# Kernel optimization log

Measured on AMD Instinct MI355X. Metric: run time of the kernel, lower is better.

The kernel has to match this reference:

```python
import jax, jax.numpy as jnp
import numpy as np

OUT = 7          # pooler output_size
RATIO = 2        # sampling_ratio
MIN_LEVEL, MAX_LEVEL = 2, 5
CANON_SIZE, CANON_LEVEL = 224.0, 4.0
SCALES = (0.25, 0.125, 0.0625, 0.03125)


def setup_inputs() -> dict:
    key = jax.random.key(0)
    ks = jax.random.split(key, 8)
    feat2 = jax.random.normal(ks[0], (2, 256, 200, 304), dtype=jnp.float32)
    feat3 = jax.random.normal(ks[1], (2, 256, 100, 152), dtype=jnp.float32)
    feat4 = jax.random.normal(ks[2], (2, 256, 50, 76), dtype=jnp.float32)
    feat5 = jax.random.normal(ks[3], (2, 256, 25, 38), dtype=jnp.float32)
    M = 1000
    imH, imW = 800.0, 1216.0
    cx = jax.random.uniform(ks[4], (M,)) * imW
    cy = jax.random.uniform(ks[5], (M,)) * imH
    wh = jax.random.uniform(ks[6], (M, 2)) * 400.0 + 8.0  # box sizes 8..408 px -> spans levels 2..5
    x0 = jnp.clip(cx - wh[:, 0] / 2, 0.0, imW - 1.0)
    x1 = jnp.clip(cx + wh[:, 0] / 2, 1.0, imW)
    y0 = jnp.clip(cy - wh[:, 1] / 2, 0.0, imH - 1.0)
    y1 = jnp.clip(cy + wh[:, 1] / 2, 1.0, imH)
    boxes = jnp.stack([x0, y0, x1, y1], axis=1).astype(jnp.float32)
    batch_idx = jax.random.randint(ks[7], (M,), 0, 2, dtype=jnp.int32)
    return {"feat2": feat2, "feat3": feat3, "feat4": feat4, "feat5": feat5,
            "boxes": boxes, "batch_idx": batch_idx}


def _assign_levels(boxes):
    # detectron2 assign_boxes_to_levels
    area = (boxes[:, 2] - boxes[:, 0]) * (boxes[:, 3] - boxes[:, 1])
    size = jnp.sqrt(area)
    lvl = jnp.floor(CANON_LEVEL + jnp.log2(size / CANON_SIZE + 1e-8))
    lvl = jnp.clip(lvl, MIN_LEVEL, MAX_LEVEL)
    return (lvl - MIN_LEVEL).astype(jnp.int32)  # [M] in 0..3


def _axis_weights(c, size):
    # torchvision roi_align bilinear clamping (per axis, separable)
    valid = ((c >= -1.0) & (c <= size)).astype(c.dtype)
    cc = jnp.maximum(c, 0.0)
    lo_f = jnp.floor(cc)
    cap = lo_f >= size - 1
    lo = jnp.where(cap, size - 1, lo_f).astype(jnp.int32)
    hi = jnp.where(cap, size - 1, lo + 1).astype(jnp.int32)
    l = jnp.where(cap, 0.0, cc - lo_f)
    return lo, hi, (1.0 - l) * valid, l * valid


def _roi_align(feat, boxes, bidx, scale):
    # feat [N,C,H,W], boxes [M,4] xyxy, aligned=True (ROIAlignV2)
    N, C, H, W = feat.shape
    M = boxes.shape[0]
    b = boxes * scale - 0.5  # aligned: shift by -0.5 after scaling
    x0, y0 = b[:, 0], b[:, 1]
    bin_w = (b[:, 2] - x0) / OUT
    bin_h = (b[:, 3] - y0) / OUT
    S = OUT * RATIO
    s = np.arange(S)
    offs = jnp.asarray((s // RATIO) + ((s % RATIO) + 0.5) / RATIO, dtype=feat.dtype)  # [S]
    ys = y0[:, None] + bin_h[:, None] * offs[None, :]  # [M,S]
    xs = x0[:, None] + bin_w[:, None] * offs[None, :]  # [M,S]
    ylo, yhi, wyl, wyh = _axis_weights(ys, H)
    xlo, xhi, wxl, wxh = _axis_weights(xs, W)

    def gather(yi, xi):
        # -> [M, S, S, C]
        return feat[bidx[:, None, None], :, yi[:, :, None], xi[:, None, :]]

    val = (gather(ylo, xlo) * (wyl[:, :, None] * wxl[:, None, :])[..., None]
         + gather(ylo, xhi) * (wyl[:, :, None] * wxh[:, None, :])[..., None]
         + gather(yhi, xlo) * (wyh[:, :, None] * wxl[:, None, :])[..., None]
         + gather(yhi, xhi) * (wyh[:, :, None] * wxh[:, None, :])[..., None])
    # average over the RATIOxRATIO sample subgrid of each output bin
    val = val.reshape(M, OUT, RATIO, OUT, RATIO, C).mean(axis=(2, 4))
    return val.transpose(0, 3, 1, 2)  # [M, C, OUT, OUT]


def reference(feat2, feat3, feat4, feat5, boxes, batch_idx):
    feats = (feat2, feat3, feat4, feat5)
    assign = _assign_levels(boxes)  # [M]
    M, C = boxes.shape[0], feat2.shape[1]
    out = jnp.zeros((M, C, OUT, OUT), dtype=feat2.dtype)
    for lvl, (f, sc) in enumerate(zip(feats, SCALES)):
        pooled = _roi_align(f, boxes, batch_idx, sc)
        out = out + pooled * (assign == lvl)[:, None, None, None].astype(out.dtype)
    return out
```

## Files before the change

kernel.cpp:

```cpp
#include <hip/hip_runtime.h>


#define NCH 256
#define POOL 7
#define NBIN 49
#define NSAMP 14
#define CAP 1152
#define WPB 4

typedef __attribute__((address_space(3))) void       as3_void;
typedef __attribute__((address_space(1))) const void as1_void;

__global__ __launch_bounds__(256, 8) void roi_align_kernel(
    const float* __restrict__ f0, const float* __restrict__ f1,
    const float* __restrict__ f2, const float* __restrict__ f3,
    const float* __restrict__ boxes, const int* __restrict__ bidx,
    float* __restrict__ out, int M)
{
    __shared__ float sF[WPB][CAP];
    __shared__ int   sXlo[WPB][NSAMP], sXhi[WPB][NSAMP];
    __shared__ int   sYlo[WPB][NSAMP], sYhi[WPB][NSAMP];
    __shared__ float sWxl[WPB][NSAMP], sWxh[WPB][NSAMP];
    __shared__ float sWyl[WPB][NSAMP], sWyh[WPB][NSAMP];

    const int lane = threadIdx.x & 63;
    const int w    = __builtin_amdgcn_readfirstlane(threadIdx.x >> 6);
    const int unit = blockIdx.x * WPB + w;
    if (unit >= M * NCH) return;
    const int m = unit >> 8;
    const int c = unit & (NCH - 1);

    float bx0 = boxes[4 * m + 0];
    float by0 = boxes[4 * m + 1];
    float bx1 = boxes[4 * m + 2];
    float by1 = boxes[4 * m + 3];

    float area = (bx1 - bx0) * (by1 - by0);
    float sz   = sqrtf(area);
    float lvlf = floorf(4.0f + log2f(sz / 224.0f + 1e-8f));
    lvlf = fminf(fmaxf(lvlf, 2.0f), 5.0f);
    int lvl = (int)lvlf - 2;

    const float* fp; int H; int W; float scale;
    if (lvl == 0)      { fp = f0; H = 200; W = 304; scale = 0.25f;    }
    else if (lvl == 1) { fp = f1; H = 100; W = 152; scale = 0.125f;   }
    else if (lvl == 2) { fp = f2; H = 50;  W = 76;  scale = 0.0625f;  }
    else               { fp = f3; H = 25;  W = 38;  scale = 0.03125f; }

    float x0 = bx0 * scale - 0.5f;
    float y0 = by0 * scale - 0.5f;
    float bin_w = (bx1 * scale - 0.5f - x0) * (1.0f / 7.0f);
    float bin_h = (by1 * scale - 0.5f - y0) * (1.0f / 7.0f);

    if (lane < 2 * NSAMP) {
        int axis = lane >= NSAMP;
        int s    = axis ? (lane - NSAMP) : lane;
        float off = (float)(s >> 1) + ((s & 1) ? 0.75f : 0.25f);
        float cv    = axis ? (y0 + bin_h * off) : (x0 + bin_w * off);
        float size  = axis ? (float)H : (float)W;
        float valid = (cv >= -1.0f && cv <= size) ? 1.0f : 0.0f;
        float cc    = fmaxf(cv, 0.0f);
        float lo_f  = floorf(cc);
        bool  cap   = lo_f >= size - 1.0f;
        int   lo    = cap ? (int)size - 1 : (int)lo_f;
        int   hi    = cap ? lo : lo + 1;
        float l     = cap ? 0.0f : (cc - lo_f);
        float wlo   = (1.0f - l) * valid;
        float whi   = l * valid;
        if (axis) { sYlo[w][s] = lo; sYhi[w][s] = hi;
                    sWyl[w][s] = wlo; sWyh[w][s] = whi; }
        else      { sXlo[w][s] = lo; sXhi[w][s] = hi;
                    sWxl[w][s] = wlo; sWxh[w][s] = whi; }
    }

    const int rx0 = sXlo[w][0];
    const int ry0 = sYlo[w][0];
    const int FW  = sXhi[w][NSAMP - 1] - rx0 + 1;
    const int FH  = sYhi[w][NSAMP - 1] - ry0 + 1;
    const int lpr = (FW + 3) >> 2;
    const int RS4 = lpr << 2;

    const size_t HW = (size_t)(H * W);
    const float* src  = fp + ((size_t)bidx[m] * NCH + c) * HW
                           + (size_t)ry0 * W + rx0;
    const float* fend = fp + (size_t)2 * NCH * HW;

    bool safe16 = (src + (size_t)(FH - 1) * W + RS4 <= fend)
               && (FH * RS4 <= CAP);

    if (safe16) {
        int rpi   = 64 / lpr;
        int iters = (FH + rpi - 1) / rpi;
        int sfy   = lane / lpr;
        int sfx4  = (lane - sfy * lpr) << 2;
        if (sfy < rpi) {
            const float* g    = src + (size_t)sfy * W + sfx4;
            const float* gmax = src + (size_t)(FH - 1) * W + sfx4;
            const size_t gstep = (size_t)rpi * W;
            char* lbase = (char*)&sF[w][0];
            const unsigned lstep = (unsigned)(rpi * RS4) * 4u;
            for (int it = 0; it < iters; ++it) {
                const float* gc = (g > gmax) ? gmax : g;
                __builtin_amdgcn_global_load_lds((as1_void*)gc,
                                                 (as3_void*)lbase, 16, 0, 0);
                g += gstep;
                lbase += lstep;
            }
        }
    } else {
        int fh2 = FH;
        if (fh2 * RS4 > CAP) fh2 = CAP / RS4;
        for (int i = lane; i < fh2 * RS4; i += 64) {
            int fy = i / RS4;
            int fx = i - fy * RS4;
            int cx = fx < FW ? fx : (FW - 1);
            sF[w][i] = src[(size_t)fy * W + cx];
        }
    }

    __builtin_amdgcn_s_waitcnt(0);
    __asm__ __volatile__("" ::: "memory");

    if (lane < NBIN) {
        int py = lane / POOL;
        int px = lane - POOL * py;
        int xa = 2 * px, xb = xa + 1;
        int xr0 = sXlo[w][xa] - rx0;
        int xr1 = sXlo[w][xb] - rx0;
        int xp0 = min(xr0 + 1, FW - 1);
        int xp1 = min(xr1 + 1, FW - 1);
        float wxl0 = sWxl[w][xa], wxh0 = sWxh[w][xa];
        float wxl1 = sWxl[w][xb], wxh1 = sWxh[w][xb];
        const float* Fb = &sF[w][0];
        float acc = 0.0f;
        #pragma unroll
        for (int sy = 0; sy < 2; ++sy) {
            int ysi = 2 * py + sy;
            int yl = sYlo[w][ysi] - ry0;
            int yh = sYhi[w][ysi] - ry0;
            float wl = sWyl[w][ysi], wh = sWyh[w][ysi];
            const float* rl = Fb + yl * RS4;
            const float* rh = Fb + yh * RS4;
            float s0 = rl[xr0] * wxl0 + rl[xp0] * wxh0
                     + rl[xr1] * wxl1 + rl[xp1] * wxh1;
            float s1 = rh[xr0] * wxl0 + rh[xp0] * wxh0
                     + rh[xr1] * wxl1 + rh[xp1] * wxh1;
            acc += wl * s0 + wh * s1;
        }
        out[(size_t)unit * NBIN + lane] = acc * 0.25f;
    }
}

extern "C" void kernel_launch(void* const* d_in, const int* in_sizes, int n_in,
                              void* d_out, int out_size, void* d_ws, size_t ws_size,
                              hipStream_t stream) {
    const float* f0    = (const float*)d_in[0];
    const float* f1    = (const float*)d_in[1];
    const float* f2    = (const float*)d_in[2];
    const float* f3    = (const float*)d_in[3];
    const float* boxes = (const float*)d_in[4];
    const int*   bidx  = (const int*)d_in[5];
    float* out = (float*)d_out;

    int M = in_sizes[4] / 4;
    int units = M * NCH;
    int blocks = (units + WPB - 1) / WPB;
    hipLaunchKernelGGL(roi_align_kernel, dim3(blocks), dim3(256), 0, stream,
                       f0, f1, f2, f3, boxes, bidx, out, M);
}
```

Baseline: 298.8 us.

## Precompute per-ROI sampling tables in a separate kernel shared by all channels

Adds a small precompute kernel that computes, once per ROI, the level, base offset, load geometry, magic-number divisors and per-sample indices and weights into a workspace table. The main kernel then reads this table instead of redoing the box math and LDS table writes for each of the 256 channels. It also switches to 32-bit offset arithmetic and multiply-shift division. The cost is an extra kernel launch plus table reads from global memory in every wave.

```diff
diff --git a/kernel.cpp b/kernel.cpp
--- a/kernel.cpp
+++ b/kernel.cpp
@@ -4,24 +4,127 @@
 #define NCH 256
 #define POOL 7
 #define NBIN 49
-#define NSAMP 14
 #define CAP 1152
 #define WPB 4
+#define TS 128
 
 typedef __attribute__((address_space(3))) void       as3_void;
 typedef __attribute__((address_space(1))) const void as1_void;
+
+__global__ __launch_bounds__(256) void roi_precompute_kernel(
+    const float* __restrict__ boxes, const int* __restrict__ bidx,
+    unsigned int* __restrict__ tab, int M)
+{
+    const int lane = threadIdx.x & 63;
+    const int m = blockIdx.x * WPB + (threadIdx.x >> 6);
+    if (m >= M) return;
+
+    float bx0 = boxes[4 * m + 0];
+    float by0 = boxes[4 * m + 1];
+    float bx1 = boxes[4 * m + 2];
+    float by1 = boxes[4 * m + 3];
+
+    float area = (bx1 - bx0) * (by1 - by0);
+    float sz   = sqrtf(area);
+    float lvlf = floorf(4.0f + log2f(sz / 224.0f + 1e-8f));
+    lvlf = fminf(fmaxf(lvlf, 2.0f), 5.0f);
+    int lvl = (int)lvlf - 2;
+
+    int H, W; float scale;
+    if (lvl == 0)      { H = 200; W = 304; scale = 0.25f;    }
+    else if (lvl == 1) { H = 100; W = 152; scale = 0.125f;   }
+    else if (lvl == 2) { H = 50;  W = 76;  scale = 0.0625f;  }
+    else               { H = 25;  W = 38;  scale = 0.03125f; }
+
+    float x0 = bx0 * scale - 0.5f;
+    float y0 = by0 * scale - 0.5f;
+    float bin_w = (bx1 * scale - 0.5f - x0) * (1.0f / 7.0f);
+    float bin_h = (by1 * scale - 0.5f - y0) * (1.0f / 7.0f);
+
+    int axis = lane >= 14;
+    int s    = axis ? (lane - 14) : lane;
+    float off = (float)(s >> 1) + ((s & 1) ? 0.75f : 0.25f);
+    float cv    = axis ? (y0 + bin_h * off) : (x0 + bin_w * off);
+    float size  = axis ? (float)H : (float)W;
+    float valid = (cv >= -1.0f && cv <= size) ? 1.0f : 0.0f;
+    float cc    = fmaxf(cv, 0.0f);
+    float lo_f  = floorf(cc);
+    bool  capd  = lo_f >= size - 1.0f;
+    int   lo    = capd ? (int)size - 1 : (int)lo_f;
+    int   hi    = capd ? lo : lo + 1;
+    float l     = capd ? 0.0f : (cc - lo_f);
+    float wlo   = (1.0f - l) * valid;
+    float whi   = l * valid;
+
+    int rx0 = __shfl(lo, 0);
+    int rxe = __shfl(hi, 13);
+    int ry0 = __shfl(lo, 14);
+    int rye = __shfl(hi, 27);
+
+    int FW  = rxe - rx0 + 1;
+    int FH  = rye - ry0 + 1;
+    int lpr = (FW + 3) >> 2;
+    int RS4 = lpr << 2;
+    int rpi = 64 / lpr;
+    int iters = (FH + rpi - 1) / rpi;
+    unsigned Mg  = (65536u   + (unsigned)lpr - 1u) / (unsigned)lpr;
+    unsigned Mg2 = (4194304u + (unsigned)RS4 - 1u) / (unsigned)RS4;
+    unsigned HW  = (unsigned)(H * W);
+    unsigned base_off = (unsigned)bidx[m] * 256u * HW
+                      + (unsigned)ry0 * (unsigned)W + (unsigned)rx0;
+    int FH2 = FH;
+    if (FH2 * RS4 > CAP) FH2 = CAP / RS4;
+    unsigned lastoff = base_off + 255u * HW
+                     + (unsigned)(FH - 1) * (unsigned)W + (unsigned)RS4;
+    int safe = (lastoff <= 2u * 256u * HW) && (FH * RS4 <= CAP);
+
+    unsigned* t = tab + (size_t)m * TS;
+    if (lane == 0) {
+        t[0]  = base_off;
+        t[1]  = (unsigned)lvl;
+        t[2]  = HW;
+        t[3]  = (unsigned)W;
+        t[4]  = (unsigned)lpr;
+        t[5]  = Mg;
+        t[6]  = (unsigned)rpi;
+        t[7]  = (unsigned)iters;
+        t[8]  = (unsigned)(rpi * W);
+        t[9]  = (unsigned)((rpi * RS4) << 2);
+        t[10] = (unsigned)((FH - 1) * W);
+        t[11] = (unsigned)safe;
+        t[12] = (unsigned)FW;
+        t[13] = (unsigned)RS4;
+        t[14] = (unsigned)FH2;
+        t[15] = Mg2;
+    }
+    if (lane < 28) {
+        if (!axis) {
+            int xr = lo - rx0;
+            int xp = min(xr + 1, FW - 1);
+            uint4 v;
+            v.x = (unsigned)xr;
+            v.y = (unsigned)xp;
+            v.z = __float_as_uint(wlo);
+            v.w = __float_as_uint(whi);
+            *(uint4*)(t + 16 + 4 * s) = v;
+        } else {
+            uint4 v;
+            v.x = (unsigned)((lo - ry0) * RS4);
+            v.y = (unsigned)((hi - ry0) * RS4);
+            v.z = __float_as_uint(wlo);
+            v.w = __float_as_uint(whi);
+            *(uint4*)(t + 72 + 4 * s) = v;
+        }
+    }
+}
 
 __global__ __launch_bounds__(256, 8) void roi_align_kernel(
     const float* __restrict__ f0, const float* __restrict__ f1,
     const float* __restrict__ f2, const float* __restrict__ f3,
-    const float* __restrict__ boxes, const int* __restrict__ bidx,
+    const unsigned int* __restrict__ tab,
     float* __restrict__ out, int M)
 {
     __shared__ float sF[WPB][CAP];
-    __shared__ int   sXlo[WPB][NSAMP], sXhi[WPB][NSAMP];
-    __shared__ int   sYlo[WPB][NSAMP], sYhi[WPB][NSAMP];
-    __shared__ float sWxl[WPB][NSAMP], sWxh[WPB][NSAMP];
-    __shared__ float sWyl[WPB][NSAMP], sWyh[WPB][NSAMP];
 
     const int lane = threadIdx.x & 63;
     const int w    = __builtin_amdgcn_readfirstlane(threadIdx.x >> 6);
@@ -30,91 +133,64 @@
     const int m = unit >> 8;
     const int c = unit & (NCH - 1);
 
-    float bx0 = boxes[4 * m + 0];
-    float by0 = boxes[4 * m + 1];
-    float bx1 = boxes[4 * m + 2];
-    float by1 = boxes[4 * m + 3];
-
-    float area = (bx1 - bx0) * (by1 - by0);
-    float sz   = sqrtf(area);
-    float lvlf = floorf(4.0f + log2f(sz / 224.0f + 1e-8f));
-    lvlf = fminf(fmaxf(lvlf, 2.0f), 5.0f);
-    int lvl = (int)lvlf - 2;
-
-    const float* fp; int H; int W; float scale;
-    if (lvl == 0)      { fp = f0; H = 200; W = 304; scale = 0.25f;    }
-    else if (lvl == 1) { fp = f1; H = 100; W = 152; scale = 0.125f;   }
-    else if (lvl == 2) { fp = f2; H = 50;  W = 76;  scale = 0.0625f;  }
-    else               { fp = f3; H = 25;  W = 38;  scale = 0.03125f; }
-
-    float x0 = bx0 * scale - 0.5f;
-    float y0 = by0 * scale - 0.5f;
-    float bin_w = (bx1 * scale - 0.5f - x0) * (1.0f / 7.0f);
-    float bin_h = (by1 * scale - 0.5f - y0) * (1.0f / 7.0f);
-
-    if (lane < 2 * NSAMP) {
-        int axis = lane >= NSAMP;
-        int s    = axis ? (lane - NSAMP) : lane;
-        float off = (float)(s >> 1) + ((s & 1) ? 0.75f : 0.25f);
-        float cv    = axis ? (y0 + bin_h * off) : (x0 + bin_w * off);
-        float size  = axis ? (float)H : (float)W;
-        float valid = (cv >= -1.0f && cv <= size) ? 1.0f : 0.0f;
-        float cc    = fmaxf(cv, 0.0f);
-        float lo_f  = floorf(cc);
-        bool  cap   = lo_f >= size - 1.0f;
-        int   lo    = cap ? (int)size - 1 : (int)lo_f;
-        int   hi    = cap ? lo : lo + 1;
-        float l     = cap ? 0.0f : (cc - lo_f);
-        float wlo   = (1.0f - l) * valid;
-        float whi   = l * valid;
-        if (axis) { sYlo[w][s] = lo; sYhi[w][s] = hi;
-                    sWyl[w][s] = wlo; sWyh[w][s] = whi; }
-        else      { sXlo[w][s] = lo; sXhi[w][s] = hi;
-                    sWxl[w][s] = wlo; sWxh[w][s] = whi; }
-    }
-
-    const int rx0 = sXlo[w][0];
-    const int ry0 = sYlo[w][0];
-    const int FW  = sXhi[w][NSAMP - 1] - rx0 + 1;
-    const int FH  = sYhi[w][NSAMP - 1] - ry0 + 1;
-    const int lpr = (FW + 3) >> 2;
-    const int RS4 = lpr << 2;
-
-    const size_t HW = (size_t)(H * W);
-    const float* src  = fp + ((size_t)bidx[m] * NCH + c) * HW
-                           + (size_t)ry0 * W + rx0;
-    const float* fend = fp + (size_t)2 * NCH * HW;
-
-    bool safe16 = (src + (size_t)(FH - 1) * W + RS4 <= fend)
-               && (FH * RS4 <= CAP);
-
-    if (safe16) {
-        int rpi   = 64 / lpr;
-        int iters = (FH + rpi - 1) / rpi;
-        int sfy   = lane / lpr;
-        int sfx4  = (lane - sfy * lpr) << 2;
+    const unsigned* t = tab + (size_t)m * TS;
+
+    const int ci = lane < NBIN ? lane : 0;
+    const int py = ci / POOL;
+    const int px = ci - POOL * py;
+    const uint4* xt = (const uint4*)(t + 16);
+    const uint4* yt = (const uint4*)(t + 72);
+    const uint4 X0 = xt[2 * px];
+    const uint4 X1 = xt[2 * px + 1];
+    const uint4 Y0 = yt[2 * py];
+    const uint4 Y1 = yt[2 * py + 1];
+
+    const uint4 s0 = *(const uint4*)(t);
+    const uint4 s1 = *(const uint4*)(t + 4);
+    const uint4 s2 = *(const uint4*)(t + 8);
+
+    const int lvl = __builtin_amdgcn_readfirstlane((int)s0.y);
+    const float* fp = (lvl == 0) ? f0 : (lvl == 1) ? f1 : (lvl == 2) ? f2 : f3;
+    const unsigned HW = s0.z;
+    const unsigned Wd = s0.w;
+    const float* src = fp + (size_t)(s0.x + (unsigned)c * HW);
+
+    const int safe = __builtin_amdgcn_readfirstlane((int)s2.w);
+    if (safe) {
+        const int lpr      = __builtin_amdgcn_readfirstlane((int)s1.x);
+        const unsigned Mg  = s1.y;
+        const int rpi      = __builtin_amdgcn_readfirstlane((int)s1.z);
+        const int iters    = __builtin_amdgcn_readfirstlane((int)s1.w);
+        const unsigned gstep  = s2.x;
+        const unsigned lstepB = __builtin_amdgcn_readfirstlane((int)s2.y);
+        const unsigned fhw    = s2.z;
+
+        int sfy  = (int)(((unsigned)lane * Mg) >> 16);
+        int sfx4 = (lane - sfy * lpr) << 2;
         if (sfy < rpi) {
-            const float* g    = src + (size_t)sfy * W + sfx4;
-            const float* gmax = src + (size_t)(FH - 1) * W + sfx4;
-            const size_t gstep = (size_t)rpi * W;
-            char* lbase = (char*)&sF[w][0];
-            const unsigned lstep = (unsigned)(rpi * RS4) * 4u;
+            const float* g    = src + (unsigned)sfy * Wd + (unsigned)sfx4;
+            const float* gmax = src + fhw + (unsigned)sfx4;
+            char* lb = (char*)&sF[w][0];
             for (int it = 0; it < iters; ++it) {
                 const float* gc = (g > gmax) ? gmax : g;
                 __builtin_amdgcn_global_load_lds((as1_void*)gc,
-                                                 (as3_void*)lbase, 16, 0, 0);
-                g += gstep;
-                lbase += lstep;
+                                                 (as3_void*)lb, 16, 0, 0);
+                g  += gstep;
+                lb += lstepB;
             }
         }
     } else {
-        int fh2 = FH;
-        if (fh2 * RS4 > CAP) fh2 = CAP / RS4;
-        for (int i = lane; i < fh2 * RS4; i += 64) {
-            int fy = i / RS4;
+        const uint4 s3 = *(const uint4*)(t + 12);
+        const int FW  = __builtin_amdgcn_readfirstlane((int)s3.x);
+        const int RS4 = __builtin_amdgcn_readfirstlane((int)s3.y);
+        const int FH2 = __builtin_amdgcn_readfirstlane((int)s3.z);
+        const unsigned Mg2 = s3.w;
+        const int tot = FH2 * RS4;
+        for (int i = lane; i < tot; i += 64) {
+            int fy = (int)(((unsigned)i * Mg2) >> 22);
             int fx = i - fy * RS4;
-            int cx = fx < FW ? fx : (FW - 1);
-            sF[w][i] = src[(size_t)fy * W + cx];
+            int cx = fx < FW ? fx : FW - 1;
+            sF[w][i] = src[(unsigned)fy * Wd + (unsigned)cx];
         }
     }
 
@@ -122,31 +198,24 @@
     __asm__ __volatile__("" ::: "memory");
 
     if (lane < NBIN) {
-        int py = lane / POOL;
-        int px = lane - POOL * py;
-        int xa = 2 * px, xb = xa + 1;
-        int xr0 = sXlo[w][xa] - rx0;
-        int xr1 = sXlo[w][xb] - rx0;
-        int xp0 = min(xr0 + 1, FW - 1);
-        int xp1 = min(xr1 + 1, FW - 1);
-        float wxl0 = sWxl[w][xa], wxh0 = sWxh[w][xa];
-        float wxl1 = sWxl[w][xb], wxh1 = sWxh[w][xb];
         const float* Fb = &sF[w][0];
-        float acc = 0.0f;
-        #pragma unroll
-        for (int sy = 0; sy < 2; ++sy) {
-            int ysi = 2 * py + sy;
-            int yl = sYlo[w][ysi] - ry0;
-            int yh = sYhi[w][ysi] - ry0;
-            float wl = sWyl[w][ysi], wh = sWyh[w][ysi];
-            const float* rl = Fb + yl * RS4;
-            const float* rh = Fb + yh * RS4;
-            float s0 = rl[xr0] * wxl0 + rl[xp0] * wxh0
-                     + rl[xr1] * wxl1 + rl[xp1] * wxh1;
-            float s1 = rh[xr0] * wxl0 + rh[xp0] * wxh0
-                     + rh[xr1] * wxl1 + rh[xp1] * wxh1;
-            acc += wl * s0 + wh * s1;
-        }
+        const unsigned xr0 = X0.x, xp0 = X0.y, xr1 = X1.x, xp1 = X1.y;
+        const float wxl0 = __uint_as_float(X0.z), wxh0 = __uint_as_float(X0.w);
+        const float wxl1 = __uint_as_float(X1.z), wxh1 = __uint_as_float(X1.w);
+        const unsigned ra = Y0.x, rb = Y0.y, rc = Y1.x, rd = Y1.y;
+
+        float a0 = Fb[ra + xr0] * wxl0 + Fb[ra + xp0] * wxh0
+                 + Fb[ra + xr1] * wxl1 + Fb[ra + xp1] * wxh1;
+        float a1 = Fb[rb + xr0] * wxl0 + Fb[rb + xp0] * wxh0
+                 + Fb[rb + xr1] * wxl1 + Fb[rb + xp1] * wxh1;
+        float a2 = Fb[rc + xr0] * wxl0 + Fb[rc + xp0] * wxh0
+                 + Fb[rc + xr1] * wxl1 + Fb[rc + xp1] * wxh1;
+        float a3 = Fb[rd + xr0] * wxl0 + Fb[rd + xp0] * wxh0
+                 + Fb[rd + xr1] * wxl1 + Fb[rd + xp1] * wxh1;
+
+        float acc = __uint_as_float(Y0.z) * a0 + __uint_as_float(Y0.w) * a1
+                  + __uint_as_float(Y1.z) * a2 + __uint_as_float(Y1.w) * a3;
+
         out[(size_t)unit * NBIN + lane] = acc * 0.25f;
     }
 }
@@ -163,8 +232,14 @@
     float* out = (float*)d_out;
 
     int M = in_sizes[4] / 4;
+    unsigned int* tab = (unsigned int*)d_ws;
+
+    int pblocks = (M + WPB - 1) / WPB;
+    hipLaunchKernelGGL(roi_precompute_kernel, dim3(pblocks), dim3(256), 0,
+                       stream, boxes, bidx, tab, M);
+
     int units = M * NCH;
     int blocks = (units + WPB - 1) / WPB;
     hipLaunchKernelGGL(roi_align_kernel, dim3(blocks), dim3(256), 0, stream,
-                       f0, f1, f2, f3, boxes, bidx, out, M);
+                       f0, f1, f2, f3, tab, out, M);
 }
```

Result: faster. 292.8 us (-2.0%).
